# Performance work log

Hardware: AMD Instinct MI355X
Metric: run time of the kernel (lower is better)

## Reference

```python
import jax, jax.numpy as jnp
import numpy as np

B, N, D = 32, 1024, 128


def setup_inputs() -> dict:
    key = jax.random.key(0)
    ks = jax.random.split(key, 8)
    scale = 0.05
    P = jax.random.normal(ks[0], (B, N, D), dtype=jnp.float32)
    w_itr_att = jax.random.normal(ks[1], (3 * D,), dtype=jnp.float32) * scale
    w1 = jax.random.normal(ks[2], (2 * D, D), dtype=jnp.float32) * scale
    w2 = jax.random.normal(ks[3], (2 * D, D), dtype=jnp.float32) * scale
    w3 = jax.random.normal(ks[4], (2 * D, D), dtype=jnp.float32) * scale
    b1 = jnp.zeros((D,), dtype=jnp.float32)
    b2 = jnp.zeros((D,), dtype=jnp.float32)
    b3 = jnp.zeros((D,), dtype=jnp.float32)
    return {"P": P, "w_itr_att": w_itr_att, "w1": w1, "w2": w2,
            "w3": w3, "b1": b1, "b2": b2, "b3": b3}


def reference(P, w_itr_att, w1, w2, w3, b1, b2, b3):
    # P: [b, n, d]
    d = P.shape[-1]
    # Original builds alphaP[b,i,:,j] = concat(P[b,j], P[b,i], P[b,j]*P[b,i])
    # and A[b,i,j] = w_itr_att . alphaP[b,i,:,j]. Decompose w to avoid the
    # O(n^2 * 3d) tensor while computing identical math.
    wa, wb, wc = w_itr_att[:d], w_itr_att[d:2 * d], w_itr_att[2 * d:]
    A = (P @ wb)[:, :, None] + (P @ wa)[:, None, :] \
        + jnp.einsum('bid,bjd->bij', P * wc, P)  # [b, n, n]
    SA = jax.nn.softmax(A, axis=-1)              # softmax over j (axis=2)
    itr_attn = jnp.einsum('bij,bjd->bid', SA, P)  # batch_dot(SA, P)
    # Fuse gate (dropout is identity at inference)
    P_concat = jnp.concatenate([P, itr_attn], axis=2)  # [b, n, 2d]
    z = jnp.tanh(P_concat @ w1 + b1)
    r = jax.nn.sigmoid(P_concat @ w2 + b2)
    f = jax.nn.sigmoid(P_concat @ w3 + b3)
    return r * P + f * z
```

## Files before the change

kernel.cpp:

```cpp
#include <hip/hip_runtime.h>
#include <math.h>

#define BB 32
#define NN 1024
#define DD 128

typedef __bf16 bf16;
typedef bf16 bf16x4 __attribute__((ext_vector_type(4)));
typedef bf16 bf16x8 __attribute__((ext_vector_type(8)));
typedef float f32x4 __attribute__((ext_vector_type(4)));
typedef float f32x16 __attribute__((ext_vector_type(16)));

#define MFMA16(a, b, c) __builtin_amdgcn_mfma_f32_16x16x32_bf16(a, b, c, 0, 0, 0)
#define MFMA32(a, b, c) __builtin_amdgcn_mfma_f32_32x32x16_bf16(a, b, c, 0, 0, 0)

__device__ inline bf16x4 swap32(bf16x4 v) {
    union { bf16x4 h; int i[2]; } u, r;
    u.h = v;
    r.i[0] = __shfl_xor(u.i[0], 32, 64);
    r.i[1] = __shfl_xor(u.i[1], 32, 64);
    return r.h;
}

__global__ __launch_bounds__(256) void k_prep(const float* __restrict__ P,
                                              const float* __restrict__ w_itr,
                                              bf16* __restrict__ Xbf,
                                              bf16* __restrict__ Pq,
                                              bf16* __restrict__ Ptp,
                                              float* __restrict__ t) {
    __shared__ bf16 Lt[128 * 72];
    int tid = threadIdx.x;
    int b = blockIdx.x >> 4, g = blockIdx.x & 15;
    int n0 = g * 64;
    int row = tid >> 2, q = tid & 3, d0 = q * 32;
    long brow = (long)b * NN + n0 + row;

    const float* src = P + brow * DD + d0;
    float r[32];
#pragma unroll
    for (int i = 0; i < 8; ++i) {
        float4 v = ((const float4*)src)[i];
        r[4 * i + 0] = v.x; r[4 * i + 1] = v.y; r[4 * i + 2] = v.z; r[4 * i + 3] = v.w;
    }
    float s = 0.f;
#pragma unroll
    for (int k = 0; k < 32; ++k) s += r[k] * w_itr[d0 + k];
    s += __shfl_xor(s, 1);
    s += __shfl_xor(s, 2);
    if (q == 0) t[brow] = s;
    const float* wc = w_itr + 2 * DD;
#pragma unroll
    for (int i = 0; i < 4; ++i) {
        bf16x8 xv, qv;
#pragma unroll
        for (int e = 0; e < 8; ++e) {
            float f = r[8 * i + e];
            xv[e] = (bf16)f;
            qv[e] = (bf16)(f * wc[d0 + 8 * i + e]);
        }
        *(bf16x8*)&Xbf[brow * 256 + d0 + 8 * i] = xv;
        *(bf16x8*)&Pq[brow * DD + d0 + 8 * i] = qv;
    }
#pragma unroll
    for (int k = 0; k < 32; ++k) Lt[(d0 + k) * 72 + row] = (bf16)r[k];
    __syncthreads();
#pragma unroll
    for (int i = 0; i < 4; ++i) {
        int idx = tid + i * 256;
        int d = idx >> 3, c = idx & 7;
        *(float4*)&Ptp[((long)b * DD + d) * NN + n0 + c * 8] =
            *(const float4*)&Lt[d * 72 + c * 8];
    }
}

__global__ __launch_bounds__(256) void k_prepw(const float* __restrict__ w1,
                                               const float* __restrict__ w2,
                                               const float* __restrict__ w3,
                                               bf16* __restrict__ WtG) {
    __shared__ float Lw[32][33];
    int bi = blockIdx.x;
    int mat = bi >> 5, rem = bi & 31;
    int kt = rem >> 2, ct = rem & 3;
    const float* wsrc = (mat == 0) ? w1 : ((mat == 1) ? w2 : w3);
    int tid = threadIdx.x;
#pragma unroll
    for (int p = 0; p < 4; ++p) {
        int idx = tid + p * 256;
        int kr = idx >> 5, c = idx & 31;
        Lw[kr][c] = wsrc[(kt * 32 + kr) * DD + ct * 32 + c];
    }
    __syncthreads();
    int colg = tid >> 3, kq = tid & 7;
    bf16x4 v;
#pragma unroll
    for (int e = 0; e < 4; ++e) v[e] = (bf16)Lw[kq * 4 + e][colg];
    *(bf16x4*)&WtG[(mat * 128 + ct * 32 + colg) * 256 + kt * 32 + kq * 4] = v;
}

__global__ __launch_bounds__(256, 2) void k_attn(bf16* __restrict__ Xbf,
                                                 const bf16* __restrict__ Pq,
                                                 const bf16* __restrict__ Ptp,
                                                 const float* __restrict__ t) {
    __shared__ __align__(16) char smem[72704];
    bf16* Kt = (bf16*)smem;
    bf16* Vt = (bf16*)(smem + 34816);
    float* tsh = (float*)(smem + 71680);
    float* lbuf = (float*)(smem + 72192);
    float* Obuf = (float*)smem;

    const int tid = threadIdx.x;
    const int w = tid >> 6, lane = tid & 63;
    const int col = lane & 31, q = lane >> 5;
    const int kh = w >> 1, rg = w & 1;
    const int b = blockIdx.x & 31, qt = blockIdx.x >> 5;
    const long qbase = (long)b * NN + qt * 64 + rg * 32;

    const bf16* KtH = Kt + kh * (64 * 136);
    const bf16* VtH = Vt + kh * (128 * 72);
    const float* tH = tsh + kh * 64;

    bf16x8 Qb[8];
#pragma unroll
    for (int c = 0; c < 8; ++c)
        Qb[c] = *(const bf16x8*)&Pq[(qbase + col) * DD + c * 16 + q * 8];

    f32x16 O[4];
#pragma unroll
    for (int mt = 0; mt < 4; ++mt)
#pragma unroll
        for (int r = 0; r < 16; ++r) O[mt][r] = 0.f;
    float lsum = 0.f;

    float4 kr[8];
    float tr = 0.f;
    auto loadK = [&](int jt) {
#pragma unroll
        for (int i = 0; i < 8; ++i) {
            int idx = tid + i * 256;
            int h = idx >> 10, rem = idx & 1023;
            int key = rem >> 4, c16 = rem & 15;
            kr[i] = *(const float4*)&Xbf[((long)b * NN + h * 512 + jt * 64 + key) * 256 + c16 * 8];
        }
        tr = (tid < 128) ? t[(long)b * NN + (tid >> 6) * 512 + jt * 64 + (tid & 63)] : 0.f;
    };

    loadK(0);
    for (int jt = 0; jt < 8; ++jt) {
        __syncthreads();
#pragma unroll
        for (int i = 0; i < 8; ++i) {
            int idx = tid + i * 256;
            int h = idx >> 10, rem = idx & 1023;
            int key = rem >> 4, c16 = rem & 15;
            *(float4*)&Kt[h * (64 * 136) + key * 136 + c16 * 8] = kr[i];
        }
        if (tid < 128) tsh[tid] = tr;
        float4 vr[8];
#pragma unroll
        for (int i = 0; i < 8; ++i) {
            int idx = tid + i * 256;
            int h = idx >> 10, rem = idx & 1023;
            int d = rem >> 3, c8 = rem & 7;
            vr[i] = *(const float4*)&Ptp[((long)b * DD + d) * NN + h * 512 + jt * 64 + c8 * 8];
        }
#pragma unroll
        for (int i = 0; i < 8; ++i) {
            int idx = tid + i * 256;
            int h = idx >> 10, rem = idx & 1023;
            int d = rem >> 3, c8 = rem & 7;
            *(float4*)&Vt[h * (128 * 72) + d * 72 + c8 * 8] = vr[i];
        }
        __syncthreads();
        if (jt < 7) loadK(jt + 1);

#pragma unroll
        for (int kt = 0; kt < 2; ++kt) {
            f32x16 S;
#pragma unroll
            for (int r = 0; r < 16; ++r) S[r] = 0.f;
#pragma unroll
            for (int c = 0; c < 8; ++c)
                S = MFMA32(*(const bf16x8*)&KtH[(kt * 32 + col) * 136 + c * 16 + q * 8],
                           Qb[c], S);
            float tqs[16];
#pragma unroll
            for (int i = 0; i < 4; ++i) {
                float4 tv = *(const float4*)&tH[kt * 32 + 8 * i + 4 * q];
                tqs[4 * i + 0] = tv.x; tqs[4 * i + 1] = tv.y;
                tqs[4 * i + 2] = tv.z; tqs[4 * i + 3] = tv.w;
            }
            float pv[16];
#pragma unroll
            for (int r = 0; r < 16; ++r) {
                float e = __expf(fminf(S[r] + tqs[r], 80.f));
                pv[r] = e;
                lsum += e;
            }
            bf16x4 Qd[4];
#pragma unroll
            for (int i = 0; i < 4; ++i)
#pragma unroll
                for (int e = 0; e < 4; ++e) Qd[i][e] = (bf16)pv[4 * i + e];
            bf16x4 sA = q ? Qd[0] : Qd[1];
            bf16x4 rA = swap32(sA);
            bf16x4 sB = q ? Qd[2] : Qd[3];
            bf16x4 rB = swap32(sB);
            bf16x4 lo0 = q ? rA : Qd[0], hi0 = q ? Qd[1] : rA;
            bf16x4 lo1 = q ? rB : Qd[2], hi1 = q ? Qd[3] : rB;
            bf16x8 f0, f1;
#pragma unroll
            for (int e = 0; e < 4; ++e) {
                f0[e] = lo0[e]; f0[4 + e] = hi0[e];
                f1[e] = lo1[e]; f1[4 + e] = hi1[e];
            }
#pragma unroll
            for (int mt = 0; mt < 4; ++mt) {
                O[mt] = MFMA32(*(const bf16x8*)&VtH[(mt * 32 + col) * 72 + kt * 32 + q * 8],
                               f0, O[mt]);
                O[mt] = MFMA32(*(const bf16x8*)&VtH[(mt * 32 + col) * 72 + kt * 32 + 16 + q * 8],
                               f1, O[mt]);
            }
        }
    }

    float l2 = lsum + __shfl_xor(lsum, 32, 64);
    if (q == 0) lbuf[(kh * 2 + rg) * 32 + col] = l2;
    __syncthreads();
    if (kh == 1) {
#pragma unroll
        for (int mt = 0; mt < 4; ++mt)
#pragma unroll
            for (int r = 0; r < 16; ++r) {
                int d = mt * 32 + (r & 3) + 8 * (r >> 2) + 4 * q;
                Obuf[(rg * 128 + d) * 36 + col] = O[mt][r];
            }
    }
    __syncthreads();
    if (kh == 0) {
        float linv = 1.f / (lbuf[(0 * 2 + rg) * 32 + col] + lbuf[(1 * 2 + rg) * 32 + col]);
#pragma unroll
        for (int mt = 0; mt < 4; ++mt)
#pragma unroll
            for (int r = 0; r < 16; ++r) {
                int d = mt * 32 + (r & 3) + 8 * (r >> 2) + 4 * q;
                int ix = (rg * 128 + d) * 36 + col;
                Obuf[ix] = (O[mt][r] + Obuf[ix]) * linv;
            }
    }
    __syncthreads();
    {
        int colg = tid & 31, rg2 = (tid >> 5) & 1, w4 = tid >> 6;
        long grow = (long)b * NN + qt * 64 + rg2 * 32 + colg;
#pragma unroll
        for (int p = 0; p < 4; ++p) {
            bf16x8 v8;
#pragma unroll
            for (int e = 0; e < 8; ++e)
                v8[e] = (bf16)Obuf[(rg2 * 128 + w4 * 32 + p * 8 + e) * 36 + colg];
            *(bf16x8*)&Xbf[grow * 256 + 128 + w4 * 32 + p * 8] = v8;
        }
    }
}

__global__ __launch_bounds__(256, 2) void k_mlp(const bf16* __restrict__ Xbf,
                                                const bf16* __restrict__ WtG,
                                                const float* __restrict__ P,
                                                const float* __restrict__ b1,
                                                const float* __restrict__ b2,
                                                const float* __restrict__ b3,
                                                float* __restrict__ out) {
    const int tid = threadIdx.x;
    const int w = tid >> 6, lane = tid & 63, ln = lane & 15, q3 = lane >> 4;
    const int rg = w & 1, ch = w >> 1;
    const long row0 = (long)blockIdx.x * 64 + rg * 32;

    bf16x8 Af[2][8];
#pragma unroll
    for (int mt = 0; mt < 2; ++mt)
#pragma unroll
        for (int kc = 0; kc < 8; ++kc)
            Af[mt][kc] = *(const bf16x8*)&Xbf[(row0 + mt * 16 + ln) * 256 + kc * 32 + q3 * 8];

    f32x4 stz[2][4], str[2][4];
#pragma unroll
    for (int mat = 0; mat < 3; ++mat) {
        f32x4 acc[2][4];
#pragma unroll
        for (int mt = 0; mt < 2; ++mt)
#pragma unroll
            for (int nt = 0; nt < 4; ++nt) acc[mt][nt] = (f32x4){0.f, 0.f, 0.f, 0.f};
#pragma unroll
        for (int kc = 0; kc < 8; ++kc)
#pragma unroll
            for (int nt = 0; nt < 4; ++nt) {
                bf16x8 Bf = *(const bf16x8*)&WtG[(mat * 128 + ch * 64 + nt * 16 + ln) * 256 +
                                                 kc * 32 + q3 * 8];
                acc[0][nt] = MFMA16(Af[0][kc], Bf, acc[0][nt]);
                acc[1][nt] = MFMA16(Af[1][kc], Bf, acc[1][nt]);
            }
        const float* bp = (mat == 0) ? b1 : ((mat == 1) ? b2 : b3);
#pragma unroll
        for (int mt = 0; mt < 2; ++mt)
#pragma unroll
            for (int nt = 0; nt < 4; ++nt) {
                int colc = ch * 64 + nt * 16 + ln;
                float bb = bp[colc];
#pragma unroll
                for (int r = 0; r < 4; ++r) {
                    float y = acc[mt][nt][r] + bb;
                    if (mat == 0) stz[mt][nt][r] = tanhf(y);
                    else if (mat == 1) str[mt][nt][r] = 1.f / (1.f + __expf(-y));
                    else {
                        float fg = 1.f / (1.f + __expf(-y));
                        long row = row0 + mt * 16 + q3 * 4 + r;
                        float p = P[row * DD + colc];
                        out[row * DD + colc] = str[mt][nt][r] * p + fg * stz[mt][nt][r];
                    }
                }
            }
    }
}

extern "C" void kernel_launch(void* const* d_in, const int* in_sizes, int n_in,
                              void* d_out, int out_size, void* d_ws, size_t ws_size,
                              hipStream_t stream) {
    const float* P     = (const float*)d_in[0];
    const float* w_itr = (const float*)d_in[1];
    const float* w1    = (const float*)d_in[2];
    const float* w2    = (const float*)d_in[3];
    const float* w3    = (const float*)d_in[4];
    const float* b1    = (const float*)d_in[5];
    const float* b2    = (const float*)d_in[6];
    const float* b3    = (const float*)d_in[7];
    float* out = (float*)d_out;

    char* wsb = (char*)d_ws;
    bf16* Xbf  = (bf16*)(wsb);
    bf16* Pq   = (bf16*)(wsb + 16777216);
    bf16* Ptp  = (bf16*)(wsb + 25165824);
    float* tws = (float*)(wsb + 33554432);
    bf16* WtG  = (bf16*)(wsb + 33685504);

    k_prep<<<dim3(BB * 16), dim3(256), 0, stream>>>(P, w_itr, Xbf, Pq, Ptp, tws);
    k_prepw<<<dim3(96), dim3(256), 0, stream>>>(w1, w2, w3, WtG);
    k_attn<<<dim3(512), dim3(256), 0, stream>>>(Xbf, Pq, Ptp, tws);
    k_mlp<<<dim3(512), dim3(256), 0, stream>>>(Xbf, WtG, P, b1, b2, b3, out);
}
```

Measured before the change: 183.9 us.

## Fuse gate MLP into attention kernel via shared-memory concat tile

The gated MLP is merged into the attention kernel. Each block writes its normalized attention output as bf16 into a shared-memory tile next to the staged P rows, then runs the three gate GEMMs straight from LDS, so the attention result no longer goes through global memory and one launch disappears. The prep kernel is also reworked to stage P through a padded fp32 LDS tile with coalesced loads, Xbf shrinks to 128 columns, and K/V prefetch is merged into one load phase. In exchange, registers and LDS pressure in the fused kernel go up, and the MLP now runs at attention's occupancy.

```diff
diff --git a/kernel.cpp b/kernel.cpp
--- a/kernel.cpp
+++ b/kernel.cpp
@@ -22,54 +22,66 @@
     return r.h;
 }
 
+#define LTS 133
 __global__ __launch_bounds__(256) void k_prep(const float* __restrict__ P,
                                               const float* __restrict__ w_itr,
                                               bf16* __restrict__ Xbf,
                                               bf16* __restrict__ Pq,
                                               bf16* __restrict__ Ptp,
                                               float* __restrict__ t) {
-    __shared__ bf16 Lt[128 * 72];
+    __shared__ float Lt[64 * LTS];
     int tid = threadIdx.x;
     int b = blockIdx.x >> 4, g = blockIdx.x & 15;
     int n0 = g * 64;
-    int row = tid >> 2, q = tid & 3, d0 = q * 32;
-    long brow = (long)b * NN + n0 + row;
-
-    const float* src = P + brow * DD + d0;
-    float r[32];
+    long base = ((long)b * NN + n0) * DD;
 #pragma unroll
     for (int i = 0; i < 8; ++i) {
-        float4 v = ((const float4*)src)[i];
-        r[4 * i + 0] = v.x; r[4 * i + 1] = v.y; r[4 * i + 2] = v.z; r[4 * i + 3] = v.w;
-    }
-    float s = 0.f;
-#pragma unroll
-    for (int k = 0; k < 32; ++k) s += r[k] * w_itr[d0 + k];
-    s += __shfl_xor(s, 1);
-    s += __shfl_xor(s, 2);
-    if (q == 0) t[brow] = s;
+        int idx = tid + i * 256;
+        int row = idx >> 5, c4 = idx & 31;
+        *(float4*)&Lt[row * LTS + c4 * 4] = *(const float4*)&P[base + row * 128 + c4 * 4];
+    }
+    __syncthreads();
+    {
+        int row = tid >> 2, q = tid & 3;
+        float s = 0.f;
+#pragma unroll
+        for (int kk = 0; kk < 32; ++kk) {
+            int k = 4 * kk + q;
+            s += Lt[row * LTS + k] * w_itr[k];
+        }
+        s += __shfl_xor(s, 1);
+        s += __shfl_xor(s, 2);
+        if (q == 0) t[(long)b * NN + n0 + row] = s;
+    }
     const float* wc = w_itr + 2 * DD;
 #pragma unroll
     for (int i = 0; i < 4; ++i) {
+        int idx = tid + i * 256;
+        int row = idx >> 4, seg = idx & 15;
+        float4 va = *(const float4*)&Lt[row * LTS + seg * 8];
+        float4 vb = *(const float4*)&Lt[row * LTS + seg * 8 + 4];
+        float4 wa4 = *(const float4*)&wc[seg * 8];
+        float4 wb4 = *(const float4*)&wc[seg * 8 + 4];
+        float fv[8] = {va.x, va.y, va.z, va.w, vb.x, vb.y, vb.z, vb.w};
+        float wv[8] = {wa4.x, wa4.y, wa4.z, wa4.w, wb4.x, wb4.y, wb4.z, wb4.w};
         bf16x8 xv, qv;
 #pragma unroll
         for (int e = 0; e < 8; ++e) {
-            float f = r[8 * i + e];
-            xv[e] = (bf16)f;
-            qv[e] = (bf16)(f * wc[d0 + 8 * i + e]);
-        }
-        *(bf16x8*)&Xbf[brow * 256 + d0 + 8 * i] = xv;
-        *(bf16x8*)&Pq[brow * DD + d0 + 8 * i] = qv;
-    }
-#pragma unroll
-    for (int k = 0; k < 32; ++k) Lt[(d0 + k) * 72 + row] = (bf16)r[k];
-    __syncthreads();
+            xv[e] = (bf16)fv[e];
+            qv[e] = (bf16)(fv[e] * wv[e]);
+        }
+        long rowg = (long)b * NN + n0 + row;
+        *(bf16x8*)&Xbf[rowg * 128 + seg * 8] = xv;
+        *(bf16x8*)&Pq[rowg * 128 + seg * 8] = qv;
+    }
 #pragma unroll
     for (int i = 0; i < 4; ++i) {
         int idx = tid + i * 256;
         int d = idx >> 3, c = idx & 7;
-        *(float4*)&Ptp[((long)b * DD + d) * NN + n0 + c * 8] =
-            *(const float4*)&Lt[d * 72 + c * 8];
+        bf16x8 v;
+#pragma unroll
+        for (int e = 0; e < 8; ++e) v[e] = (bf16)Lt[(c * 8 + e) * LTS + d];
+        *(bf16x8*)&Ptp[((long)b * DD + d) * NN + n0 + c * 8] = v;
     }
 }
 
@@ -97,32 +109,36 @@
     *(bf16x4*)&WtG[(mat * 128 + ct * 32 + colg) * 256 + kt * 32 + kq * 4] = v;
 }
 
-__global__ __launch_bounds__(256, 2) void k_attn(bf16* __restrict__ Xbf,
+__global__ __launch_bounds__(256, 2) void k_attn(const bf16* __restrict__ Xbf,
                                                  const bf16* __restrict__ Pq,
                                                  const bf16* __restrict__ Ptp,
-                                                 const float* __restrict__ t) {
+                                                 const float* __restrict__ t,
+                                                 const bf16* __restrict__ WtG,
+                                                 const float* __restrict__ P,
+                                                 const float* __restrict__ b1,
+                                                 const float* __restrict__ b2,
+                                                 const float* __restrict__ b3,
+                                                 float* __restrict__ out) {
     __shared__ __align__(16) char smem[72704];
     bf16* Kt = (bf16*)smem;
     bf16* Vt = (bf16*)(smem + 34816);
     float* tsh = (float*)(smem + 71680);
     float* lbuf = (float*)(smem + 72192);
     float* Obuf = (float*)smem;
+    bf16* Xsh = (bf16*)(smem + 34816);
 
     const int tid = threadIdx.x;
     const int w = tid >> 6, lane = tid & 63;
     const int col = lane & 31, q = lane >> 5;
     const int kh = w >> 1, rg = w & 1;
     const int b = blockIdx.x & 31, qt = blockIdx.x >> 5;
-    const long qbase = (long)b * NN + qt * 64 + rg * 32;
-
-    const bf16* KtH = Kt + kh * (64 * 136);
-    const bf16* VtH = Vt + kh * (128 * 72);
-    const float* tH = tsh + kh * 64;
+    const long qrow0 = (long)b * NN + qt * 64;
+    const long qbase = qrow0 + rg * 32;
 
     bf16x8 Qb[8];
 #pragma unroll
     for (int c = 0; c < 8; ++c)
-        Qb[c] = *(const bf16x8*)&Pq[(qbase + col) * DD + c * 16 + q * 8];
+        Qb[c] = *(const bf16x8*)&Pq[(qbase + col) * 128 + c * 16 + q * 8];
 
     f32x16 O[4];
 #pragma unroll
@@ -131,48 +147,38 @@
         for (int r = 0; r < 16; ++r) O[mt][r] = 0.f;
     float lsum = 0.f;
 
-    float4 kr[8];
+    float4 kr[8], vr[8];
     float tr = 0.f;
-    auto loadK = [&](int jt) {
+    auto loadKV = [&](int jt) {
 #pragma unroll
         for (int i = 0; i < 8; ++i) {
             int idx = tid + i * 256;
             int h = idx >> 10, rem = idx & 1023;
-            int key = rem >> 4, c16 = rem & 15;
-            kr[i] = *(const float4*)&Xbf[((long)b * NN + h * 512 + jt * 64 + key) * 256 + c16 * 8];
+            kr[i] = *(const float4*)&Xbf[((long)b * NN + h * 512 + jt * 64 + (rem >> 4)) * 128 +
+                                         (rem & 15) * 8];
+            vr[i] = *(const float4*)&Ptp[((long)b * DD + (rem >> 3)) * NN + h * 512 + jt * 64 +
+                                         (rem & 7) * 8];
         }
         tr = (tid < 128) ? t[(long)b * NN + (tid >> 6) * 512 + jt * 64 + (tid & 63)] : 0.f;
     };
 
-    loadK(0);
+    loadKV(0);
     for (int jt = 0; jt < 8; ++jt) {
         __syncthreads();
 #pragma unroll
         for (int i = 0; i < 8; ++i) {
             int idx = tid + i * 256;
             int h = idx >> 10, rem = idx & 1023;
-            int key = rem >> 4, c16 = rem & 15;
-            *(float4*)&Kt[h * (64 * 136) + key * 136 + c16 * 8] = kr[i];
+            *(float4*)&Kt[h * (64 * 136) + (rem >> 4) * 136 + (rem & 15) * 8] = kr[i];
+            *(float4*)&Vt[h * (128 * 72) + (rem >> 3) * 72 + (rem & 7) * 8] = vr[i];
         }
         if (tid < 128) tsh[tid] = tr;
-        float4 vr[8];
-#pragma unroll
-        for (int i = 0; i < 8; ++i) {
-            int idx = tid + i * 256;
-            int h = idx >> 10, rem = idx & 1023;
-            int d = rem >> 3, c8 = rem & 7;
-            vr[i] = *(const float4*)&Ptp[((long)b * DD + d) * NN + h * 512 + jt * 64 + c8 * 8];
-        }
-#pragma unroll
-        for (int i = 0; i < 8; ++i) {
-            int idx = tid + i * 256;
-            int h = idx >> 10, rem = idx & 1023;
-            int d = rem >> 3, c8 = rem & 7;
-            *(float4*)&Vt[h * (128 * 72) + d * 72 + c8 * 8] = vr[i];
-        }
         __syncthreads();
-        if (jt < 7) loadK(jt + 1);
-
+        if (jt < 7) loadKV(jt + 1);
+
+        const bf16* KtH = Kt + kh * (64 * 136);
+        const bf16* VtH = Vt + kh * (128 * 72);
+        const float* tH = tsh + kh * 64;
 #pragma unroll
         for (int kt = 0; kt < 2; ++kt) {
             f32x16 S;
@@ -232,8 +238,17 @@
 #pragma unroll
             for (int r = 0; r < 16; ++r) {
                 int d = mt * 32 + (r & 3) + 8 * (r >> 2) + 4 * q;
-                Obuf[(rg * 128 + d) * 36 + col] = O[mt][r];
-            }
+                Obuf[(rg * 128 + d) * 33 + col] = O[mt][r];
+            }
+    } else {
+        int tl = tid;
+#pragma unroll
+        for (int i = 0; i < 8; ++i) {
+            int idx = tl + i * 128;
+            int row = idx >> 4, seg = idx & 15;
+            *(bf16x8*)&Xsh[row * 264 + seg * 8] =
+                *(const bf16x8*)&Xbf[(qrow0 + row) * 128 + seg * 8];
+        }
     }
     __syncthreads();
     if (kh == 0) {
@@ -243,44 +258,14 @@
 #pragma unroll
             for (int r = 0; r < 16; ++r) {
                 int d = mt * 32 + (r & 3) + 8 * (r >> 2) + 4 * q;
-                int ix = (rg * 128 + d) * 36 + col;
-                Obuf[ix] = (O[mt][r] + Obuf[ix]) * linv;
-            }
-    }
-    __syncthreads();
-    {
-        int colg = tid & 31, rg2 = (tid >> 5) & 1, w4 = tid >> 6;
-        long grow = (long)b * NN + qt * 64 + rg2 * 32 + colg;
-#pragma unroll
-        for (int p = 0; p < 4; ++p) {
-            bf16x8 v8;
-#pragma unroll
-            for (int e = 0; e < 8; ++e)
-                v8[e] = (bf16)Obuf[(rg2 * 128 + w4 * 32 + p * 8 + e) * 36 + colg];
-            *(bf16x8*)&Xbf[grow * 256 + 128 + w4 * 32 + p * 8] = v8;
-        }
-    }
-}
-
-__global__ __launch_bounds__(256, 2) void k_mlp(const bf16* __restrict__ Xbf,
-                                                const bf16* __restrict__ WtG,
-                                                const float* __restrict__ P,
-                                                const float* __restrict__ b1,
-                                                const float* __restrict__ b2,
-                                                const float* __restrict__ b3,
-                                                float* __restrict__ out) {
-    const int tid = threadIdx.x;
-    const int w = tid >> 6, lane = tid & 63, ln = lane & 15, q3 = lane >> 4;
-    const int rg = w & 1, ch = w >> 1;
-    const long row0 = (long)blockIdx.x * 64 + rg * 32;
-
-    bf16x8 Af[2][8];
-#pragma unroll
-    for (int mt = 0; mt < 2; ++mt)
-#pragma unroll
-        for (int kc = 0; kc < 8; ++kc)
-            Af[mt][kc] = *(const bf16x8*)&Xbf[(row0 + mt * 16 + ln) * 256 + kc * 32 + q3 * 8];
-
+                float v = (O[mt][r] + Obuf[(rg * 128 + d) * 33 + col]) * linv;
+                Xsh[(rg * 32 + col) * 264 + 128 + d] = (bf16)v;
+            }
+    }
+    __syncthreads();
+
+    const int ln = lane & 15, q3 = lane >> 4;
+    const int ch = w >> 1, rg2 = w & 1;
     f32x4 stz[2][4], str[2][4];
 #pragma unroll
     for (int mat = 0; mat < 3; ++mat) {
@@ -290,14 +275,17 @@
 #pragma unroll
             for (int nt = 0; nt < 4; ++nt) acc[mt][nt] = (f32x4){0.f, 0.f, 0.f, 0.f};
 #pragma unroll
-        for (int kc = 0; kc < 8; ++kc)
+        for (int kc = 0; kc < 8; ++kc) {
+            bf16x8 Af0 = *(const bf16x8*)&Xsh[(rg2 * 32 + ln) * 264 + kc * 32 + q3 * 8];
+            bf16x8 Af1 = *(const bf16x8*)&Xsh[(rg2 * 32 + 16 + ln) * 264 + kc * 32 + q3 * 8];
 #pragma unroll
             for (int nt = 0; nt < 4; ++nt) {
                 bf16x8 Bf = *(const bf16x8*)&WtG[(mat * 128 + ch * 64 + nt * 16 + ln) * 256 +
                                                  kc * 32 + q3 * 8];
-                acc[0][nt] = MFMA16(Af[0][kc], Bf, acc[0][nt]);
-                acc[1][nt] = MFMA16(Af[1][kc], Bf, acc[1][nt]);
-            }
+                acc[0][nt] = MFMA16(Af0, Bf, acc[0][nt]);
+                acc[1][nt] = MFMA16(Af1, Bf, acc[1][nt]);
+            }
+        }
         const float* bp = (mat == 0) ? b1 : ((mat == 1) ? b2 : b3);
 #pragma unroll
         for (int mt = 0; mt < 2; ++mt)
@@ -312,7 +300,7 @@
                     else if (mat == 1) str[mt][nt][r] = 1.f / (1.f + __expf(-y));
                     else {
                         float fg = 1.f / (1.f + __expf(-y));
-                        long row = row0 + mt * 16 + q3 * 4 + r;
+                        long row = qrow0 + rg2 * 32 + mt * 16 + q3 * 4 + r;
                         float p = P[row * DD + colc];
                         out[row * DD + colc] = str[mt][nt][r] * p + fg * stz[mt][nt][r];
                     }
@@ -336,13 +324,12 @@
 
     char* wsb = (char*)d_ws;
     bf16* Xbf  = (bf16*)(wsb);
-    bf16* Pq   = (bf16*)(wsb + 16777216);
-    bf16* Ptp  = (bf16*)(wsb + 25165824);
-    float* tws = (float*)(wsb + 33554432);
-    bf16* WtG  = (bf16*)(wsb + 33685504);
+    bf16* Pq   = (bf16*)(wsb + 8388608);
+    bf16* Ptp  = (bf16*)(wsb + 16777216);
+    float* tws = (float*)(wsb + 25165824);
+    bf16* WtG  = (bf16*)(wsb + 25296896);
 
     k_prep<<<dim3(BB * 16), dim3(256), 0, stream>>>(P, w_itr, Xbf, Pq, Ptp, tws);
     k_prepw<<<dim3(96), dim3(256), 0, stream>>>(w1, w2, w3, WtG);
-    k_attn<<<dim3(512), dim3(256), 0, stream>>>(Xbf, Pq, Ptp, tws);
-    k_mlp<<<dim3(512), dim3(256), 0, stream>>>(Xbf, WtG, P, b1, b2, b3, out);
-}
+    k_attn<<<dim3(512), dim3(256), 0, stream>>>(Xbf, Pq, Ptp, tws, WtG, P, b1, b2, b3, out);
+}
```

New measurement: 198.0 us. 7.7% more time.
